# Kernel tuning notes

Hardware: AMD Instinct MI355X
Metric: run time of the kernel (lower is better)

## Reference

```python
import jax, jax.numpy as jnp
import numpy as np

N_NODES = 100000
N_EDGES = 1600000
IN_F = 64
HID = 64
NUM_GRAPHS = 256


def _lin(x, W, b):
    # Linear: x [N, in] @ W [in, out] + b [out]
    return x @ W + b


def _spect_conv(x, src, dst, W, b):
    # SpectConv, K=1, selfconn=False, edge_attr == 1:
    # h[i] = sum_{(j->i) in E} x[j];  out = h @ W + b
    h = jax.ops.segment_sum(x[src], dst, num_segments=N_NODES)
    return h @ W + b


def setup_inputs() -> dict:
    key = jax.random.key(0)
    ks = jax.random.split(key, 40)
    inp = {
        "x": jax.random.normal(ks[0], (N_NODES, IN_F), dtype=jnp.float32),
        "edge_index": jax.random.randint(ks[1], (2, N_EDGES), 0, N_NODES, dtype=jnp.int64),
        "batch": jnp.sort(jax.random.randint(ks[2], (N_NODES,), 0, NUM_GRAPHS, dtype=jnp.int64)),
    }
    i = 3
    def mk(shape):
        nonlocal i
        w = jax.random.normal(ks[i], shape, dtype=jnp.float32) * 0.05
        i += 1
        return w
    for l, fin in ((1, IN_F), (2, HID), (3, HID)):
        inp[f"conv{l}_w"] = mk((fin, HID)); inp[f"conv{l}_b"] = mk((HID,))
        for j in (1, 2, 3):
            inp[f"fc{l}{j}_w"] = mk((fin, HID)); inp[f"fc{l}{j}_b"] = mk((HID,))
    inp["fc1_w"] = mk((HID, 10)); inp["fc1_b"] = mk((10,))
    inp["fc2_w"] = mk((10, 1)); inp["fc2_b"] = mk((1,))
    return inp


def reference(x, edge_index, batch,
              conv1_w, conv1_b, fc11_w, fc11_b, fc12_w, fc12_b, fc13_w, fc13_b,
              conv2_w, conv2_b, fc21_w, fc21_b, fc22_w, fc22_b, fc23_w, fc23_b,
              conv3_w, conv3_b, fc31_w, fc31_b, fc32_w, fc32_b, fc33_w, fc33_b,
              fc1_w, fc1_b, fc2_w, fc2_b):
    src, dst = edge_index[0], edge_index[1]

    def layer(h, fa_w, fa_b, cw, cb, fb_w, fb_b, fc_w, fc_b):
        return jax.nn.relu(_lin(h, fa_w, fa_b)
                           + _spect_conv(h, src, dst, cw, cb)
                           + _lin(h, fb_w, fb_b) * _lin(h, fc_w, fc_b))

    h = layer(x, fc11_w, fc11_b, conv1_w, conv1_b, fc12_w, fc12_b, fc13_w, fc13_b)
    h = layer(h, fc21_w, fc21_b, conv2_w, conv2_b, fc22_w, fc22_b, fc23_w, fc23_b)
    h = layer(h, fc31_w, fc31_b, conv3_w, conv3_b, fc32_w, fc32_b, fc33_w, fc33_b)

    # global_mean_pool over graph ids
    sums = jax.ops.segment_sum(h, batch, num_segments=NUM_GRAPHS)
    cnts = jax.ops.segment_sum(jnp.ones((h.shape[0], 1), h.dtype), batch, num_segments=NUM_GRAPHS)
    pooled = sums / jnp.maximum(cnts, 1.0)

    g = _lin(pooled, fc1_w, fc1_b)
    return _lin(g, fc2_w, fc2_b)  # [NUM_GRAPHS, 1]
```

## Files before the change

kernel.cpp:

```cpp
#include <hip/hip_runtime.h>
#include <hip/hip_fp16.h>

#define NN 100000
#define NE 1600000
#define NG 256
#define NPB 64
#define LAYER_GRID 512

#define BSH 9
#define NBKT ((NN + 511) / 512)
#define CAP 9216
#define TILE_A 4096
#define NBLK_A ((NE + TILE_A - 1) / TILE_A)

typedef _Float16 f16x8 __attribute__((ext_vector_type(8)));
typedef float f32x4 __attribute__((ext_vector_type(4)));

__device__ __forceinline__ uint2 f4_to_h16(float4 o) {
    __half2 lo = __floats2half2_rn(o.x, o.y);
    __half2 hi = __floats2half2_rn(o.z, o.w);
    uint2 u;
    u.x = *(unsigned int*)&lo;
    u.y = *(unsigned int*)&hi;
    return u;
}

__global__ __launch_bounds__(256) void cvt_kernel(const float* __restrict__ in,
                                                  __half* __restrict__ out) {
    const int i = blockIdx.x * 256 + threadIdx.x;
    const int n4 = NN * 64 / 4;
    if (i < n4) {
        float4 v = ((const float4*)in)[i];
        ((uint2*)out)[i] = f4_to_h16(v);
    }
}

__global__ __launch_bounds__(256) void initcur_kernel(int* __restrict__ gcur) {
    int t = threadIdx.x;
    if (t < NBKT) gcur[t] = t * CAP;
}

__global__ __launch_bounds__(256) void binA_kernel(const int* __restrict__ src,
                                                   const int* __restrict__ dst,
                                                   int* __restrict__ gcur,
                                                   unsigned int* __restrict__ binned)
{
    __shared__ int hist[NBKT];
    __shared__ int cnt2[NBKT];
    __shared__ int lexcl[NBKT];
    __shared__ int base[NBKT];
    __shared__ int s[256];
    __shared__ unsigned int buf[TILE_A];
    __shared__ unsigned char bkt8[TILE_A];

    const int t = threadIdx.x;
    const int e0 = blockIdx.x * TILE_A;
    const int nedge = min(TILE_A, NE - e0);

    if (t < NBKT) { hist[t] = 0; cnt2[t] = 0; }
    __syncthreads();

    for (int j = t; j < nedge; j += 256)
        atomicAdd(&hist[dst[e0 + j] >> BSH], 1);
    __syncthreads();

    s[t] = (t < NBKT) ? hist[t] : 0;
    __syncthreads();
    for (int off = 1; off < 256; off <<= 1) {
        int u = (t >= off) ? s[t - off] : 0;
        __syncthreads();
        s[t] += u;
        __syncthreads();
    }
    if (t < NBKT) {
        lexcl[t] = s[t] - hist[t];
        if (hist[t] > 0) base[t] = atomicAdd(&gcur[t], hist[t]);
    }
    __syncthreads();

    for (int j = t; j < nedge; j += 256) {
        const int d = dst[e0 + j];
        const int sv = src[e0 + j];
        const int b = d >> BSH;
        const int r = atomicAdd(&cnt2[b], 1);
        const int idx = lexcl[b] + r;
        buf[idx] = ((unsigned int)sv << BSH) | (unsigned int)(d & 511);
        bkt8[idx] = (unsigned char)b;
    }
    __syncthreads();

    for (int j = t; j < nedge; j += 256) {
        const int b = bkt8[j];
        binned[base[b] + (j - lexcl[b])] = buf[j];
    }
}

__global__ __launch_bounds__(256) void bscan_kernel(const int* __restrict__ gcur,
                                                    int* __restrict__ bbase,
                                                    int* __restrict__ rs)
{
    __shared__ int s[256];
    const int t = threadIdx.x;
    const int sz = (t < NBKT) ? (gcur[t] - t * CAP) : 0;
    s[t] = sz;
    __syncthreads();
    for (int off = 1; off < 256; off <<= 1) {
        int u = (t >= off) ? s[t - off] : 0;
        __syncthreads();
        s[t] += u;
        __syncthreads();
    }
    if (t < NBKT) bbase[t] = s[t] - sz;
    if (t == 0) rs[NN] = NE;
}

__global__ __launch_bounds__(256) void binB_kernel(const unsigned int* __restrict__ binned,
                                                   const int* __restrict__ gcur,
                                                   const int* __restrict__ bbase,
                                                   int* __restrict__ csr,
                                                   int* __restrict__ rs)
{
    __shared__ int cnt[512];
    __shared__ int excl[512];
    __shared__ int cnt2[512];
    __shared__ int psum[256];
    __shared__ unsigned int buf[CAP];

    const int b = blockIdx.x;
    const int t = threadIdx.x;
    const int sz = gcur[b] - b * CAP;
    const int gb = bbase[b];
    const unsigned int* bp = binned + b * CAP;

    cnt[t] = 0; cnt[t + 256] = 0;
    cnt2[t] = 0; cnt2[t + 256] = 0;
    __syncthreads();

    for (int j = t; j < sz; j += 256) {
        const unsigned int v = bp[j];
        buf[j] = v;
        atomicAdd(&cnt[v & 511], 1);
    }
    __syncthreads();

    const int c0 = cnt[2 * t], c1 = cnt[2 * t + 1];
    psum[t] = c0 + c1;
    __syncthreads();
    for (int off = 1; off < 256; off <<= 1) {
        int u = (t >= off) ? psum[t - off] : 0;
        __syncthreads();
        psum[t] += u;
        __syncthreads();
    }
    const int pe = psum[t] - (c0 + c1);
    excl[2 * t] = pe;
    excl[2 * t + 1] = pe + c0;
    __syncthreads();

    const int node0 = b << BSH;
    for (int l = t; l < 512; l += 256) {
        const int node = node0 + l;
        if (node < NN) rs[node] = gb + excl[l];
    }

    for (int j = t; j < sz; j += 256) {
        const unsigned int v = buf[j];
        const int l = v & 511;
        const int r = atomicAdd(&cnt2[l], 1);
        csr[gb + excl[l] + r] = (int)(v >> BSH);
    }
}

__device__ __forceinline__ void accu8(float* a8, uint4 u) {
    const __half2* hp = (const __half2*)&u;
    #pragma unroll
    for (int q = 0; q < 4; ++q) {
        float2 f = __half22float2(hp[q]);
        a8[2 * q] += f.x; a8[2 * q + 1] += f.y;
    }
}

__global__ __launch_bounds__(512, 4) void layer_kernel(
    const __half* __restrict__ h_in, __half* __restrict__ h_out,
    const int* __restrict__ csr, const int* __restrict__ rs,
    const float* __restrict__ Wa, const float* __restrict__ ba,
    const float* __restrict__ Wc, const float* __restrict__ bc,
    const float* __restrict__ Wb, const float* __restrict__ bb,
    const float* __restrict__ Wd, const float* __restrict__ bd)
{
    __shared__ _Float16 sX1[64][72];
    __shared__ _Float16 sX2[64][72];
    __shared__ _Float16 sW[4][64][72];

    const int tid = threadIdx.x;

    for (int e = tid; e < 4096; e += 512) {
        const int k = e >> 6, n = e & 63;
        sW[0][n][k] = (_Float16)Wa[e];
        sW[1][n][k] = (_Float16)Wc[e];
        sW[2][n][k] = (_Float16)Wb[e];
        sW[3][n][k] = (_Float16)Wd[e];
    }

    const int slot = tid >> 3;
    const int fg8  = tid & 7;

    const int w   = tid >> 6;
    const int l   = tid & 63;
    const int lr  = l & 15;
    const int kh  = l >> 4;
    const int nt  = w & 3;
    const int mt0 = (w >> 2) * 16;
    const int col = nt * 16 + lr;
    const float bA = ba[col], bC = bc[col], bB = bb[col], bD = bd[col];

    const int npass = (NN + NPB - 1) / NPB;
    for (int g = blockIdx.x; g < npass; g += gridDim.x) {
        const int node0 = g * NPB;

        const int node = node0 + slot;
        uint4 hreg = make_uint4(0u, 0u, 0u, 0u);
        float a8[8] = {0.f, 0.f, 0.f, 0.f, 0.f, 0.f, 0.f, 0.f};
        if (node < NN) {
            hreg = *(const uint4*)(h_in + node * 64 + fg8 * 8);
            int e = rs[node];
            const int ee = rs[node + 1];
            for (; e < ee; e += 8) {
                const int rem = ee - e;
                const int s0 = csr[e];
                const int s1 = rem > 1 ? csr[e + 1] : s0;
                const int s2 = rem > 2 ? csr[e + 2] : s0;
                const int s3 = rem > 3 ? csr[e + 3] : s0;
                const int s4 = rem > 4 ? csr[e + 4] : s0;
                const int s5 = rem > 5 ? csr[e + 5] : s0;
                const int s6 = rem > 6 ? csr[e + 6] : s0;
                const int s7 = rem > 7 ? csr[e + 7] : s0;
                const uint4 u0 = *(const uint4*)(h_in + s0 * 64 + fg8 * 8);
                const uint4 u1 = *(const uint4*)(h_in + s1 * 64 + fg8 * 8);
                const uint4 u2 = *(const uint4*)(h_in + s2 * 64 + fg8 * 8);
                const uint4 u3 = *(const uint4*)(h_in + s3 * 64 + fg8 * 8);
                const uint4 u4 = *(const uint4*)(h_in + s4 * 64 + fg8 * 8);
                const uint4 u5 = *(const uint4*)(h_in + s5 * 64 + fg8 * 8);
                const uint4 u6 = *(const uint4*)(h_in + s6 * 64 + fg8 * 8);
                const uint4 u7 = *(const uint4*)(h_in + s7 * 64 + fg8 * 8);
                accu8(a8, u0);
                if (rem > 1) accu8(a8, u1);
                if (rem > 2) accu8(a8, u2);
                if (rem > 3) accu8(a8, u3);
                if (rem > 4) accu8(a8, u4);
                if (rem > 5) accu8(a8, u5);
                if (rem > 6) accu8(a8, u6);
                if (rem > 7) accu8(a8, u7);
            }
        }
        __syncthreads();

        *(uint4*)&sX1[slot][fg8 * 8] = hreg;
        union { _Float16 h[8]; uint4 u; } cv;
        #pragma unroll
        for (int j = 0; j < 8; ++j) cv.h[j] = (_Float16)a8[j];
        *(uint4*)&sX2[slot][fg8 * 8] = cv.u;
        __syncthreads();

        f32x4 accA1 = {0.f,0.f,0.f,0.f}, accC1 = {0.f,0.f,0.f,0.f};
        f32x4 accB1 = {0.f,0.f,0.f,0.f}, accD1 = {0.f,0.f,0.f,0.f};
        f32x4 accA2 = {0.f,0.f,0.f,0.f}, accC2 = {0.f,0.f,0.f,0.f};
        f32x4 accB2 = {0.f,0.f,0.f,0.f}, accD2 = {0.f,0.f,0.f,0.f};
        #pragma unroll
        for (int kk = 0; kk < 2; ++kk) {
            const int ko = kk * 32 + kh * 8;
            const f16x8 wba = *(const f16x8*)&sW[0][col][ko];
            const f16x8 wbc = *(const f16x8*)&sW[1][col][ko];
            const f16x8 wbb = *(const f16x8*)&sW[2][col][ko];
            const f16x8 wbd = *(const f16x8*)&sW[3][col][ko];
            const f16x8 a1r0 = *(const f16x8*)&sX1[mt0 + lr][ko];
            const f16x8 a2r0 = *(const f16x8*)&sX2[mt0 + lr][ko];
            const f16x8 a1r1 = *(const f16x8*)&sX1[mt0 + 32 + lr][ko];
            const f16x8 a2r1 = *(const f16x8*)&sX2[mt0 + 32 + lr][ko];
            accA1 = __builtin_amdgcn_mfma_f32_16x16x32_f16(a1r0, wba, accA1, 0, 0, 0);
            accC1 = __builtin_amdgcn_mfma_f32_16x16x32_f16(a2r0, wbc, accC1, 0, 0, 0);
            accB1 = __builtin_amdgcn_mfma_f32_16x16x32_f16(a1r0, wbb, accB1, 0, 0, 0);
            accD1 = __builtin_amdgcn_mfma_f32_16x16x32_f16(a1r0, wbd, accD1, 0, 0, 0);
            accA2 = __builtin_amdgcn_mfma_f32_16x16x32_f16(a1r1, wba, accA2, 0, 0, 0);
            accC2 = __builtin_amdgcn_mfma_f32_16x16x32_f16(a2r1, wbc, accC2, 0, 0, 0);
            accB2 = __builtin_amdgcn_mfma_f32_16x16x32_f16(a1r1, wbb, accB2, 0, 0, 0);
            accD2 = __builtin_amdgcn_mfma_f32_16x16x32_f16(a1r1, wbd, accD2, 0, 0, 0);
        }

        #pragma unroll
        for (int r = 0; r < 4; ++r) {
            int row = mt0 + kh * 4 + r;
            int nd  = node0 + row;
            if (nd < NN) {
                float o = fmaxf((accA1[r] + bA) + (accC1[r] + bC) +
                                (accB1[r] + bB) * (accD1[r] + bD), 0.f);
                h_out[nd * 64 + col] = __float2half(o);
            }
            row += 32; nd += 32;
            if (nd < NN) {
                float o = fmaxf((accA2[r] + bA) + (accC2[r] + bC) +
                                (accB2[r] + bB) * (accD2[r] + bD), 0.f);
                h_out[nd * 64 + col] = __float2half(o);
            }
        }
    }
}

__global__ __launch_bounds__(256) void pool_mlp_kernel(
    const __half* __restrict__ h, const int* __restrict__ batch,
    const float* __restrict__ w1, const float* __restrict__ b1,
    const float* __restrict__ w2, const float* __restrict__ b2,
    float* __restrict__ out)
{
    const int g = blockIdx.x;
    const int t = threadIdx.x;
    int lo = 0, hi = NN;
    while (lo < hi) { int m = (lo + hi) >> 1; if (batch[m] < g) lo = m + 1; else hi = m; }
    const int start = lo;
    hi = NN;
    while (lo < hi) { int m = (lo + hi) >> 1; if (batch[m] < g + 1) lo = m + 1; else hi = m; }
    const int end = lo;

    const int f = t & 63, wsub = t >> 6;
    float sum = 0.f;
    for (int n = start + wsub; n < end; n += 4) sum += __half2float(h[n * 64 + f]);
    __shared__ float red[4][64];
    red[wsub][f] = sum;
    __syncthreads();
    __shared__ float pooled[64];
    if (t < 64) {
        float tot = red[0][t] + red[1][t] + red[2][t] + red[3][t];
        pooled[t] = tot / fmaxf((float)(end - start), 1.f);
    }
    __syncthreads();
    __shared__ float y10[10];
    if (t < 10) {
        float acc = b1[t];
        for (int k = 0; k < 64; ++k) acc = fmaf(pooled[k], w1[k * 10 + t], acc);
        y10[t] = acc;
    }
    __syncthreads();
    if (t == 0) {
        float acc = b2[0];
        for (int j = 0; j < 10; ++j) acc = fmaf(y10[j], w2[j], acc);
        out[g] = acc;
    }
}

extern "C" void kernel_launch(void* const* d_in, const int* in_sizes, int n_in,
                              void* d_out, int out_size, void* d_ws, size_t ws_size,
                              hipStream_t stream) {
    const float* x    = (const float*)d_in[0];
    const int* ei     = (const int*)d_in[1];
    const int* batch  = (const int*)d_in[2];
    const int* src    = ei;
    const int* dstv   = ei + NE;

    char* ws     = (char*)d_ws;
    __half* hX16 = (__half*)(ws);
    __half* hA16 = (__half*)(ws + 12800000);
    int* csr     = (int*)(ws + 25600000);
    int* rs      = (int*)(ws + 32000000);
    unsigned int* binned = (unsigned int*)(ws + 32500000);
    int* gcur    = (int*)(ws + 39800000);
    int* bbase   = (int*)(ws + 39800000 + 1024);

    initcur_kernel<<<1, 256, 0, stream>>>(gcur);
    binA_kernel<<<NBLK_A, 256, 0, stream>>>(src, dstv, gcur, binned);
    bscan_kernel<<<1, 256, 0, stream>>>(gcur, bbase, rs);
    binB_kernel<<<NBKT, 256, 0, stream>>>(binned, gcur, bbase, csr, rs);
    cvt_kernel<<<(NN * 64 / 4 + 255) / 256, 256, 0, stream>>>(x, hX16);

    auto f = [&](int i) { return (const float*)d_in[i]; };
    layer_kernel<<<LAYER_GRID, 512, 0, stream>>>(hX16, hA16, csr, rs,
        f(5), f(6), f(3), f(4), f(7), f(8), f(9), f(10));
    layer_kernel<<<LAYER_GRID, 512, 0, stream>>>(hA16, hX16, csr, rs,
        f(13), f(14), f(11), f(12), f(15), f(16), f(17), f(18));
    layer_kernel<<<LAYER_GRID, 512, 0, stream>>>(hX16, hA16, csr, rs,
        f(21), f(22), f(19), f(20), f(23), f(24), f(25), f(26));

    pool_mlp_kernel<<<NG, 256, 0, stream>>>(hA16, batch,
        f(27), f(28), f(29), f(30), (float*)d_out);
}
```

Before: 217.2 us.

## Preconvert weights once, hold them in registers, stage CSR indices in LDS

A new kernel transposes and converts each layer's four weight matrices to fp16 once, and the layer kernel loads them straight into registers instead of building a shared-memory copy in every block. Blocks shrink to 256 threads and 32 nodes each, with a larger grid, so each wave owns a 16-column slice. Each pass first stages the block's contiguous CSR neighbour indices into LDS so the gather reads them from there, falling back to global memory when they overflow. This costs extra kernel launches, one more barrier per pass and more register pressure.

```diff
diff --git a/kernel.cpp b/kernel.cpp
--- a/kernel.cpp
+++ b/kernel.cpp
@@ -4,8 +4,9 @@
 #define NN 100000
 #define NE 1600000
 #define NG 256
-#define NPB 64
-#define LAYER_GRID 512
+#define NPB 32
+#define LAYER_GRID 2048
+#define SIDX 1280
 
 #define BSH 9
 #define NBKT ((NN + 511) / 512)
@@ -32,6 +33,21 @@
     if (i < n4) {
         float4 v = ((const float4*)in)[i];
         ((uint2*)out)[i] = f4_to_h16(v);
+    }
+}
+
+__global__ __launch_bounds__(256) void wprep_kernel(const float* __restrict__ Wa,
+                                                    const float* __restrict__ Wc,
+                                                    const float* __restrict__ Wb,
+                                                    const float* __restrict__ Wd,
+                                                    __half* __restrict__ out) {
+    const int i = blockIdx.x * 256 + threadIdx.x;
+    if (i < 16384) {
+        const int m = i >> 12;
+        const int e = i & 4095;
+        const int n = e >> 6, k = e & 63;
+        const float* W = (m == 0) ? Wa : (m == 1) ? Wc : (m == 2) ? Wb : Wd;
+        out[m * 4096 + n * 64 + k] = __float2half(W[k * 64 + n]);
     }
 }
 
@@ -180,27 +196,18 @@
     }
 }
 
-__global__ __launch_bounds__(512, 4) void layer_kernel(
+__global__ __launch_bounds__(256) void layer_kernel(
     const __half* __restrict__ h_in, __half* __restrict__ h_out,
     const int* __restrict__ csr, const int* __restrict__ rs,
-    const float* __restrict__ Wa, const float* __restrict__ ba,
-    const float* __restrict__ Wc, const float* __restrict__ bc,
-    const float* __restrict__ Wb, const float* __restrict__ bb,
-    const float* __restrict__ Wd, const float* __restrict__ bd)
+    const __half* __restrict__ wt,
+    const float* __restrict__ ba, const float* __restrict__ bc,
+    const float* __restrict__ bb, const float* __restrict__ bd)
 {
-    __shared__ _Float16 sX1[64][72];
-    __shared__ _Float16 sX2[64][72];
-    __shared__ _Float16 sW[4][64][72];
+    __shared__ _Float16 sX1[NPB][72];
+    __shared__ _Float16 sX2[NPB][72];
+    __shared__ int sIdx[SIDX];
 
     const int tid = threadIdx.x;
-
-    for (int e = tid; e < 4096; e += 512) {
-        const int k = e >> 6, n = e & 63;
-        sW[0][n][k] = (_Float16)Wa[e];
-        sW[1][n][k] = (_Float16)Wc[e];
-        sW[2][n][k] = (_Float16)Wb[e];
-        sW[3][n][k] = (_Float16)Wd[e];
-    }
 
     const int slot = tid >> 3;
     const int fg8  = tid & 7;
@@ -209,32 +216,53 @@
     const int l   = tid & 63;
     const int lr  = l & 15;
     const int kh  = l >> 4;
-    const int nt  = w & 3;
-    const int mt0 = (w >> 2) * 16;
-    const int col = nt * 16 + lr;
+    const int col = w * 16 + lr;
+
+    const _Float16* wtf = (const _Float16*)wt;
+    f16x8 wrA0 = *(const f16x8*)&wtf[0 * 4096 + col * 64 + 0 * 32 + kh * 8];
+    f16x8 wrA1 = *(const f16x8*)&wtf[0 * 4096 + col * 64 + 1 * 32 + kh * 8];
+    f16x8 wrC0 = *(const f16x8*)&wtf[1 * 4096 + col * 64 + 0 * 32 + kh * 8];
+    f16x8 wrC1 = *(const f16x8*)&wtf[1 * 4096 + col * 64 + 1 * 32 + kh * 8];
+    f16x8 wrB0 = *(const f16x8*)&wtf[2 * 4096 + col * 64 + 0 * 32 + kh * 8];
+    f16x8 wrB1 = *(const f16x8*)&wtf[2 * 4096 + col * 64 + 1 * 32 + kh * 8];
+    f16x8 wrD0 = *(const f16x8*)&wtf[3 * 4096 + col * 64 + 0 * 32 + kh * 8];
+    f16x8 wrD1 = *(const f16x8*)&wtf[3 * 4096 + col * 64 + 1 * 32 + kh * 8];
     const float bA = ba[col], bC = bc[col], bB = bb[col], bD = bd[col];
 
     const int npass = (NN + NPB - 1) / NPB;
     for (int g = blockIdx.x; g < npass; g += gridDim.x) {
         const int node0 = g * NPB;
+        const int e0 = rs[node0];
+        const int eN = rs[min(node0 + NPB, NN)];
+        const int staged = min(eN - e0, SIDX);
+
+        __syncthreads();
+        for (int j = tid; j < staged; j += 256) sIdx[j] = csr[e0 + j];
+        __syncthreads();
 
         const int node = node0 + slot;
         uint4 hreg = make_uint4(0u, 0u, 0u, 0u);
         float a8[8] = {0.f, 0.f, 0.f, 0.f, 0.f, 0.f, 0.f, 0.f};
         if (node < NN) {
             hreg = *(const uint4*)(h_in + node * 64 + fg8 * 8);
-            int e = rs[node];
-            const int ee = rs[node + 1];
-            for (; e < ee; e += 8) {
-                const int rem = ee - e;
-                const int s0 = csr[e];
-                const int s1 = rem > 1 ? csr[e + 1] : s0;
-                const int s2 = rem > 2 ? csr[e + 2] : s0;
-                const int s3 = rem > 3 ? csr[e + 3] : s0;
-                const int s4 = rem > 4 ? csr[e + 4] : s0;
-                const int s5 = rem > 5 ? csr[e + 5] : s0;
-                const int s6 = rem > 6 ? csr[e + 6] : s0;
-                const int s7 = rem > 7 ? csr[e + 7] : s0;
+            const int rsn = rs[node];
+            const int ne  = rs[node + 1] - rsn;
+            const int le  = rsn - e0;
+            for (int q = 0; q < ne; q += 8) {
+                const int rem = ne - q;
+                const int jb = le + q;
+                auto gi = [&](int i) {
+                    const int jr = jb + i;
+                    return (jr < staged) ? sIdx[jr] : csr[e0 + jr];
+                };
+                const int s0 = gi(0);
+                const int s1 = rem > 1 ? gi(1) : s0;
+                const int s2 = rem > 2 ? gi(2) : s0;
+                const int s3 = rem > 3 ? gi(3) : s0;
+                const int s4 = rem > 4 ? gi(4) : s0;
+                const int s5 = rem > 5 ? gi(5) : s0;
+                const int s6 = rem > 6 ? gi(6) : s0;
+                const int s7 = rem > 7 ? gi(7) : s0;
                 const uint4 u0 = *(const uint4*)(h_in + s0 * 64 + fg8 * 8);
                 const uint4 u1 = *(const uint4*)(h_in + s1 * 64 + fg8 * 8);
                 const uint4 u2 = *(const uint4*)(h_in + s2 * 64 + fg8 * 8);
@@ -253,7 +281,6 @@
                 if (rem > 7) accu8(a8, u7);
             }
         }
-        __syncthreads();
 
         *(uint4*)&sX1[slot][fg8 * 8] = hreg;
         union { _Float16 h[8]; uint4 u; } cv;
@@ -269,34 +296,34 @@
         #pragma unroll
         for (int kk = 0; kk < 2; ++kk) {
             const int ko = kk * 32 + kh * 8;
-            const f16x8 wba = *(const f16x8*)&sW[0][col][ko];
-            const f16x8 wbc = *(const f16x8*)&sW[1][col][ko];
-            const f16x8 wbb = *(const f16x8*)&sW[2][col][ko];
-            const f16x8 wbd = *(const f16x8*)&sW[3][col][ko];
-            const f16x8 a1r0 = *(const f16x8*)&sX1[mt0 + lr][ko];
-            const f16x8 a2r0 = *(const f16x8*)&sX2[mt0 + lr][ko];
-            const f16x8 a1r1 = *(const f16x8*)&sX1[mt0 + 32 + lr][ko];
-            const f16x8 a2r1 = *(const f16x8*)&sX2[mt0 + 32 + lr][ko];
-            accA1 = __builtin_amdgcn_mfma_f32_16x16x32_f16(a1r0, wba, accA1, 0, 0, 0);
-            accC1 = __builtin_amdgcn_mfma_f32_16x16x32_f16(a2r0, wbc, accC1, 0, 0, 0);
-            accB1 = __builtin_amdgcn_mfma_f32_16x16x32_f16(a1r0, wbb, accB1, 0, 0, 0);
-            accD1 = __builtin_amdgcn_mfma_f32_16x16x32_f16(a1r0, wbd, accD1, 0, 0, 0);
-            accA2 = __builtin_amdgcn_mfma_f32_16x16x32_f16(a1r1, wba, accA2, 0, 0, 0);
-            accC2 = __builtin_amdgcn_mfma_f32_16x16x32_f16(a2r1, wbc, accC2, 0, 0, 0);
-            accB2 = __builtin_amdgcn_mfma_f32_16x16x32_f16(a1r1, wbb, accB2, 0, 0, 0);
-            accD2 = __builtin_amdgcn_mfma_f32_16x16x32_f16(a1r1, wbd, accD2, 0, 0, 0);
+            const f16x8 wa = kk ? wrA1 : wrA0;
+            const f16x8 wc = kk ? wrC1 : wrC0;
+            const f16x8 wb = kk ? wrB1 : wrB0;
+            const f16x8 wd = kk ? wrD1 : wrD0;
+            const f16x8 a1r0 = *(const f16x8*)&sX1[lr][ko];
+            const f16x8 a2r0 = *(const f16x8*)&sX2[lr][ko];
+            const f16x8 a1r1 = *(const f16x8*)&sX1[16 + lr][ko];
+            const f16x8 a2r1 = *(const f16x8*)&sX2[16 + lr][ko];
+            accA1 = __builtin_amdgcn_mfma_f32_16x16x32_f16(a1r0, wa, accA1, 0, 0, 0);
+            accC1 = __builtin_amdgcn_mfma_f32_16x16x32_f16(a2r0, wc, accC1, 0, 0, 0);
+            accB1 = __builtin_amdgcn_mfma_f32_16x16x32_f16(a1r0, wb, accB1, 0, 0, 0);
+            accD1 = __builtin_amdgcn_mfma_f32_16x16x32_f16(a1r0, wd, accD1, 0, 0, 0);
+            accA2 = __builtin_amdgcn_mfma_f32_16x16x32_f16(a1r1, wa, accA2, 0, 0, 0);
+            accC2 = __builtin_amdgcn_mfma_f32_16x16x32_f16(a2r1, wc, accC2, 0, 0, 0);
+            accB2 = __builtin_amdgcn_mfma_f32_16x16x32_f16(a1r1, wb, accB2, 0, 0, 0);
+            accD2 = __builtin_amdgcn_mfma_f32_16x16x32_f16(a1r1, wd, accD2, 0, 0, 0);
         }
 
         #pragma unroll
         for (int r = 0; r < 4; ++r) {
-            int row = mt0 + kh * 4 + r;
+            int row = kh * 4 + r;
             int nd  = node0 + row;
             if (nd < NN) {
                 float o = fmaxf((accA1[r] + bA) + (accC1[r] + bC) +
                                 (accB1[r] + bB) * (accD1[r] + bD), 0.f);
                 h_out[nd * 64 + col] = __float2half(o);
             }
-            row += 32; nd += 32;
+            nd += 16;
             if (nd < NN) {
                 float o = fmaxf((accA2[r] + bA) + (accC2[r] + bC) +
                                 (accB2[r] + bB) * (accD2[r] + bD), 0.f);
@@ -364,6 +391,7 @@
     unsigned int* binned = (unsigned int*)(ws + 32500000);
     int* gcur    = (int*)(ws + 39800000);
     int* bbase   = (int*)(ws + 39800000 + 1024);
+    __half* wt   = (__half*)(ws + 39810000);
 
     initcur_kernel<<<1, 256, 0, stream>>>(gcur);
     binA_kernel<<<NBLK_A, 256, 0, stream>>>(src, dstv, gcur, binned);
@@ -372,12 +400,16 @@
     cvt_kernel<<<(NN * 64 / 4 + 255) / 256, 256, 0, stream>>>(x, hX16);
 
     auto f = [&](int i) { return (const float*)d_in[i]; };
-    layer_kernel<<<LAYER_GRID, 512, 0, stream>>>(hX16, hA16, csr, rs,
-        f(5), f(6), f(3), f(4), f(7), f(8), f(9), f(10));
-    layer_kernel<<<LAYER_GRID, 512, 0, stream>>>(hA16, hX16, csr, rs,
-        f(13), f(14), f(11), f(12), f(15), f(16), f(17), f(18));
-    layer_kernel<<<LAYER_GRID, 512, 0, stream>>>(hX16, hA16, csr, rs,
-        f(21), f(22), f(19), f(20), f(23), f(24), f(25), f(26));
+    wprep_kernel<<<64, 256, 0, stream>>>(f(5),  f(3),  f(7),  f(9),  wt);
+    wprep_kernel<<<64, 256, 0, stream>>>(f(13), f(11), f(15), f(17), wt + 16384);
+    wprep_kernel<<<64, 256, 0, stream>>>(f(21), f(19), f(23), f(25), wt + 32768);
+
+    layer_kernel<<<LAYER_GRID, 256, 0, stream>>>(hX16, hA16, csr, rs,
+        wt,         f(6), f(4), f(8), f(10));
+    layer_kernel<<<LAYER_GRID, 256, 0, stream>>>(hA16, hX16, csr, rs,
+        wt + 16384, f(14), f(12), f(16), f(18));
+    layer_kernel<<<LAYER_GRID, 256, 0, stream>>>(hX16, hA16, csr, rs,
+        wt + 32768, f(22), f(20), f(24), f(26));
 
     pool_mlp_kernel<<<NG, 256, 0, stream>>>(hA16, batch,
         f(27), f(28), f(29), f(30), (float*)d_out);
```

Measured after the change: 228.4 us. +5.2%, slower.
